# Kernel optimization log

Measured on AMD Instinct MI355X. Metric: run time of the kernel, lower is better.

Reference implementation:

```python
import jax, jax.numpy as jnp
import numpy as np

D_MODEL = 512
N_HEADS = 8
D_K = D_MODEL // N_HEADS


def setup_inputs() -> dict:
    key = jax.random.key(0)
    ks = jax.random.split(key, 11)
    B, L, D = 2, 4096, D_MODEL
    s = 1.0 / np.sqrt(D)
    return {
        "q": jax.random.normal(ks[0], (B, L, D), jnp.float32),
        "k": jax.random.normal(ks[1], (B, L, D), jnp.float32),
        "v": jax.random.normal(ks[2], (B, L, D), jnp.float32),
        "Wq": jax.random.normal(ks[3], (D, D), jnp.float32) * s,
        "bq": jnp.zeros((D,), jnp.float32),
        "Wk": jax.random.normal(ks[4], (D, D), jnp.float32) * s,
        "bk": jnp.zeros((D,), jnp.float32),
        "Wv": jax.random.normal(ks[5], (D, D), jnp.float32) * s,
        "bv": jnp.zeros((D,), jnp.float32),
        "Wo": jax.random.normal(ks[6], (D, D), jnp.float32) * s,
        "bo": jnp.zeros((D,), jnp.float32),
    }


def reference(q, k, v, Wq, bq, Wk, bk, Wv, bv, Wo, bo):
    B, L, D = q.shape
    H, dk = N_HEADS, D_K
    # projections -> [B, H, L, dk]
    qh = (q @ Wq + bq).reshape(B, L, H, dk).transpose(0, 2, 1, 3)
    kh = (k @ Wk + bk).reshape(B, -1, H, dk).transpose(0, 2, 1, 3)
    vh = (v @ Wv + bv).reshape(B, -1, H, dk).transpose(0, 2, 1, 3)
    scores = jnp.einsum("bhqd,bhkd->bhqk", qh, kh) / jnp.sqrt(jnp.float32(dk))
    attn = jax.nn.softmax(scores, axis=-1)  # dropout: eval-mode identity
    ctx = jnp.einsum("bhqk,bhkd->bhqd", attn, vh)
    ctx = ctx.transpose(0, 2, 1, 3).reshape(B, L, D)
    return ctx @ Wo + bo
```

## Files before the change

### kernel.cpp

```cpp
#include <hip/hip_runtime.h>
#include <hip/hip_bf16.h>

#define NB 2
#define NL 4096
#define ND 512
#define NH 8
#define NDK 64
#define NM (NB * NL)
#define QSCALE 0.18033688011112042f

typedef short bf16x8_t __attribute__((ext_vector_type(8)));
typedef float f32x4_t __attribute__((ext_vector_type(4)));

static __device__ __forceinline__ unsigned short f2bs(float f) {
  union { float f; unsigned u; } c; c.f = f;
  unsigned r = c.u + 0x7fffu + ((c.u >> 16) & 1u);
  return (unsigned short)(r >> 16);
}
static __device__ __forceinline__ float bs2f(unsigned short s) {
  union { unsigned u; float f; } c; c.u = ((unsigned)s) << 16; return c.f;
}
static __device__ __forceinline__ unsigned pk_bf16(float a, float b) {
  union { __hip_bfloat162 h; unsigned u; } c;
  c.h = __float22bfloat162_rn(make_float2(a, b));
  return c.u;
}

__global__ __launch_bounds__(256)
void round3_kernel(const float* __restrict__ s0, const float* __restrict__ s1,
                   const float* __restrict__ s2, unsigned short* __restrict__ d0,
                   unsigned short* __restrict__ d1, unsigned short* __restrict__ d2)
{
  const float* s = blockIdx.y == 0 ? s0 : (blockIdx.y == 1 ? s1 : s2);
  unsigned short* d = blockIdx.y == 0 ? d0 : (blockIdx.y == 1 ? d1 : d2);
  const size_t i = ((size_t)blockIdx.x * 256 + threadIdx.x) * 8;
  const float4 f0 = *(const float4*)(s + i);
  const float4 f1 = *(const float4*)(s + i + 4);
  uint4 o;
  o.x = pk_bf16(f0.x, f0.y);
  o.y = pk_bf16(f0.z, f0.w);
  o.z = pk_bf16(f1.x, f1.y);
  o.w = pk_bf16(f1.z, f1.w);
  *(uint4*)(d + i) = o;
}

struct WArgs {
  const float* W[4];
  unsigned short* Th[4];
  unsigned short* Tl[4];
};
__global__ __launch_bounds__(256)
void wsplit_kernel(WArgs a)
{
  const int z = blockIdx.z;
  const float* __restrict__ W = a.W[z];
  const int tid = threadIdx.x;
  const int n = blockIdx.x * 64 + (tid & 63);
  const int kb = blockIdx.y * 64 + (tid >> 6) * 16;
  unsigned short h[16], l[16];
#pragma unroll
  for (int u = 0; u < 16; ++u) {
    const float x = W[(size_t)(kb + u) * ND + n];
    h[u] = f2bs(x);
    l[u] = f2bs(x - bs2f(h[u]));
  }
  unsigned wh[8], wl[8];
#pragma unroll
  for (int p = 0; p < 8; ++p) {
    wh[p] = (unsigned)h[2 * p] | ((unsigned)h[2 * p + 1] << 16);
    wl[p] = (unsigned)l[2 * p] | ((unsigned)l[2 * p + 1] << 16);
  }
  unsigned short* th = a.Th[z] + (size_t)n * ND + kb;
  unsigned short* tl = a.Tl[z] + (size_t)n * ND + kb;
  *(uint4*)th = make_uint4(wh[0], wh[1], wh[2], wh[3]);
  *(uint4*)(th + 8) = make_uint4(wh[4], wh[5], wh[6], wh[7]);
  *(uint4*)tl = make_uint4(wl[0], wl[1], wl[2], wl[3]);
  *(uint4*)(tl + 8) = make_uint4(wl[4], wl[5], wl[6], wl[7]);
}

template <bool ASPLIT, bool HEADOUT>
__device__ __forceinline__ void gemm_core(
    const unsigned short* __restrict__ Ahi, const unsigned short* __restrict__ Alo,
    const unsigned short* __restrict__ Bh, const unsigned short* __restrict__ Bl,
    const float* __restrict__ bias, unsigned short* __restrict__ outH,
    float* __restrict__ outF, int m0, int n0, float scale)
{
  __shared__ unsigned short AH[128][36];
  __shared__ unsigned short AL[ASPLIT ? 128 : 1][36];
  __shared__ unsigned short BHs[128][36];
  __shared__ unsigned short BLs[128][36];

  const int tid = threadIdx.x;
  const int lane = tid & 63, w = tid >> 6;
  const int m = lane & 15, quad = lane >> 4;
  const int r = tid >> 1, hf = (tid & 1) * 16;

  const unsigned short* aRow = Ahi + (size_t)(m0 + r) * ND + hf;
  const unsigned short* alRow = ASPLIT ? (Alo + (size_t)(m0 + r) * ND + hf) : nullptr;
  const unsigned short* bhRow = Bh + (size_t)(n0 + r) * ND + hf;
  const unsigned short* blRow = Bl + (size_t)(n0 + r) * ND + hf;

  uint4 ra0 = *(const uint4*)(aRow);
  uint4 ra1 = *(const uint4*)(aRow + 8);
  uint4 rl0, rl1;
  if constexpr (ASPLIT) {
    rl0 = *(const uint4*)(alRow);
    rl1 = *(const uint4*)(alRow + 8);
  }
  uint4 rbh0 = *(const uint4*)(bhRow);
  uint4 rbh1 = *(const uint4*)(bhRow + 8);
  uint4 rbl0 = *(const uint4*)(blRow);
  uint4 rbl1 = *(const uint4*)(blRow + 8);

  f32x4_t acc[2][8];
#pragma unroll
  for (int i = 0; i < 2; ++i)
#pragma unroll
    for (int j = 0; j < 8; ++j) acc[i][j] = (f32x4_t){0.f, 0.f, 0.f, 0.f};

  for (int k0 = 0; k0 < ND; k0 += 32) {
    __syncthreads();
    *(uint4*)&AH[r][hf] = ra0;
    *(uint4*)&AH[r][hf + 8] = ra1;
    if constexpr (ASPLIT) {
      *(uint4*)&AL[r][hf] = rl0;
      *(uint4*)&AL[r][hf + 8] = rl1;
    }
    *(uint4*)&BHs[r][hf] = rbh0;
    *(uint4*)&BHs[r][hf + 8] = rbh1;
    *(uint4*)&BLs[r][hf] = rbl0;
    *(uint4*)&BLs[r][hf + 8] = rbl1;
    if (k0 + 32 < ND) {
      const int kn = k0 + 32;
      ra0 = *(const uint4*)(aRow + kn);
      ra1 = *(const uint4*)(aRow + kn + 8);
      if constexpr (ASPLIT) {
        rl0 = *(const uint4*)(alRow + kn);
        rl1 = *(const uint4*)(alRow + kn + 8);
      }
      rbh0 = *(const uint4*)(bhRow + kn);
      rbh1 = *(const uint4*)(bhRow + kn + 8);
      rbl0 = *(const uint4*)(blRow + kn);
      rbl1 = *(const uint4*)(blRow + kn + 8);
    }
    __syncthreads();

    bf16x8_t ah[2], al[2];
#pragma unroll
    for (int i = 0; i < 2; ++i) {
      ah[i] = *(const bf16x8_t*)&AH[w * 32 + 16 * i + m][quad * 8];
      if constexpr (ASPLIT) al[i] = *(const bf16x8_t*)&AL[w * 32 + 16 * i + m][quad * 8];
    }
#pragma unroll
    for (int j = 0; j < 8; ++j) {
      const bf16x8_t bhj = *(const bf16x8_t*)&BHs[16 * j + m][quad * 8];
      const bf16x8_t blj = *(const bf16x8_t*)&BLs[16 * j + m][quad * 8];
#pragma unroll
      for (int i = 0; i < 2; ++i) {
        acc[i][j] = __builtin_amdgcn_mfma_f32_16x16x32_bf16(ah[i], bhj, acc[i][j], 0, 0, 0);
        acc[i][j] = __builtin_amdgcn_mfma_f32_16x16x32_bf16(ah[i], blj, acc[i][j], 0, 0, 0);
        if constexpr (ASPLIT)
          acc[i][j] = __builtin_amdgcn_mfma_f32_16x16x32_bf16(al[i], bhj, acc[i][j], 0, 0, 0);
      }
    }
  }

#pragma unroll
  for (int i = 0; i < 2; ++i)
#pragma unroll
    for (int rr = 0; rr < 4; ++rr) {
      const int mg = m0 + w * 32 + 16 * i + quad * 4 + rr;
#pragma unroll
      for (int j = 0; j < 8; ++j) {
        const int n = n0 + 16 * j + m;
        const float c = (acc[i][j][rr] + bias[n]) * scale;
        if constexpr (HEADOUT) {
          const int b = mg >> 12, l = mg & (NL - 1);
          const int h = n >> 6, d = n & (NDK - 1);
          outH[(((size_t)(b * NH + h)) * NL + l) * NDK + d] = f2bs(c);
        } else {
          outF[(size_t)mg * ND + n] = c;
        }
      }
    }
}

struct ProjArgs {
  const unsigned short* A[3];
  const unsigned short* Bh[3];
  const unsigned short* Bl[3];
  const float* bias[3];
  unsigned short* out[3];
  float scale[3];
};
__global__ __launch_bounds__(256, 2)
void gemm_proj_kernel(ProjArgs a)
{
  const int z = blockIdx.z;
  gemm_core<false, true>(a.A[z], nullptr, a.Bh[z], a.Bl[z], a.bias[z], a.out[z],
                         nullptr, blockIdx.x * 128, blockIdx.y * 128, a.scale[z]);
}
__global__ __launch_bounds__(256, 2)
void gemm_out_kernel(const unsigned short* __restrict__ Ahi,
                     const unsigned short* __restrict__ Alo,
                     const unsigned short* __restrict__ Bh,
                     const unsigned short* __restrict__ Bl,
                     const float* __restrict__ bias, float* __restrict__ out)
{
  gemm_core<true, false>(Ahi, Alo, Bh, Bl, bias, nullptr, out,
                         blockIdx.x * 128, blockIdx.y * 128, 1.0f);
}

__global__ __launch_bounds__(256)
void vtrans_kernel(const unsigned short* __restrict__ src, unsigned short* __restrict__ dst)
{
  __shared__ unsigned short T[64][74];
  const int tid = threadIdx.x;
  const int bh = blockIdx.x >> 6;
  const int lt = blockIdx.x & 63;
  const unsigned short* s = src + ((size_t)bh * NL + lt * 64) * NDK;
  const int r = tid >> 2, c = (tid & 3) * 16;
  *(uint4*)&T[r][c] = *(const uint4*)(s + (size_t)r * NDK + c);
  *(uint4*)&T[r][c + 8] = *(const uint4*)(s + (size_t)r * NDK + c + 8);
  __syncthreads();
  const int d = tid >> 2, l0 = (tid & 3) * 16;
  unsigned short e[16];
#pragma unroll
  for (int u = 0; u < 16; ++u) e[u] = T[l0 + u][d];
  uint4 u0, u1;
  u0.x = (unsigned)e[0] | ((unsigned)e[1] << 16);
  u0.y = (unsigned)e[2] | ((unsigned)e[3] << 16);
  u0.z = (unsigned)e[4] | ((unsigned)e[5] << 16);
  u0.w = (unsigned)e[6] | ((unsigned)e[7] << 16);
  u1.x = (unsigned)e[8] | ((unsigned)e[9] << 16);
  u1.y = (unsigned)e[10] | ((unsigned)e[11] << 16);
  u1.z = (unsigned)e[12] | ((unsigned)e[13] << 16);
  u1.w = (unsigned)e[14] | ((unsigned)e[15] << 16);
  unsigned short* dp = dst + (size_t)bh * NDK * NL + (size_t)d * NL + lt * 64 + l0;
  *(uint4*)dp = u0;
  *(uint4*)(dp + 8) = u1;
}

__global__ __launch_bounds__(256, 4)
void attn_kernel(const unsigned short* __restrict__ qh, const unsigned short* __restrict__ kh,
                 const unsigned short* __restrict__ vt_g, float* __restrict__ op,
                 float* __restrict__ lp)
{
  __shared__ unsigned short Ks[64][72];
  __shared__ unsigned short Vt[64][72];
  __shared__ unsigned Pt[64][67];

  const int tid = threadIdx.x;
  const int w = tid >> 6;
  const int lane = tid & 63;
  const int m = lane & 15;
  const int quad = lane >> 4;

  const int bid = blockIdx.x;
  const int half = bid & 1;
  const int qt = (bid >> 1) & 31;
  const int bh = bid >> 6;
  const int kt0 = half * 32, kt1 = kt0 + 32;
  const unsigned short* qb = qh + (size_t)bh * NL * NDK;
  const unsigned short* kb = kh + (size_t)bh * NL * NDK;
  const unsigned short* vb = vt_g + (size_t)bh * NDK * NL;

  bf16x8_t aq[2][2];
#pragma unroll
  for (int mt = 0; mt < 2; ++mt) {
    const unsigned short* qsrc =
        qb + (size_t)(qt * 128 + w * 32 + mt * 16 + m) * NDK + quad * 8;
    aq[mt][0] = *(const bf16x8_t*)(qsrc);
    aq[mt][1] = *(const bf16x8_t*)(qsrc + 32);
  }

  const short ob = (short)0x3F80;
  const bf16x8_t ones = {ob, ob, ob, ob, ob, ob, ob, ob};

  f32x4_t o[2][4];
#pragma unroll
  for (int mt = 0; mt < 2; ++mt)
#pragma unroll
    for (int nt = 0; nt < 4; ++nt) o[mt][nt] = (f32x4_t){0.f, 0.f, 0.f, 0.f};
  f32x4_t ol[2];
  ol[0] = (f32x4_t){0.f, 0.f, 0.f, 0.f};
  ol[1] = (f32x4_t){0.f, 0.f, 0.f, 0.f};

  const int kr = tid >> 2;
  const int kc = (tid & 3) * 16;

  uint4 pk0, pk1, pv0, pv1;
  {
    const unsigned short* ksrc = kb + (size_t)(kt0 * 64 + kr) * NDK + kc;
    pk0 = *(const uint4*)ksrc;
    pk1 = *(const uint4*)(ksrc + 8);
    const unsigned short* vsrc = vb + (size_t)kr * NL + kt0 * 64 + kc;
    pv0 = *(const uint4*)vsrc;
    pv1 = *(const uint4*)(vsrc + 8);
  }

  for (int kt = kt0; kt < kt1; ++kt) {
    __syncthreads();
    *(uint4*)&Ks[kr][kc] = pk0;
    *(uint4*)&Ks[kr][kc + 8] = pk1;
    *(uint4*)&Vt[kr][kc] = pv0;
    *(uint4*)&Vt[kr][kc + 8] = pv1;
    if (kt + 1 < kt1) {
      const unsigned short* ksrc = kb + (size_t)((kt + 1) * 64 + kr) * NDK + kc;
      pk0 = *(const uint4*)ksrc;
      pk1 = *(const uint4*)(ksrc + 8);
      const unsigned short* vsrc = vb + (size_t)kr * NL + (kt + 1) * 64 + kc;
      pv0 = *(const uint4*)vsrc;
      pv1 = *(const uint4*)(vsrc + 8);
    }
    __syncthreads();

#pragma unroll
    for (int nt = 0; nt < 4; ++nt) {
      const bf16x8_t b0 = *(const bf16x8_t*)&Ks[16 * nt + m][quad * 8];
      const bf16x8_t b1 = *(const bf16x8_t*)&Ks[16 * nt + m][quad * 8 + 32];
      f32x4_t s0 = (f32x4_t){0.f, 0.f, 0.f, 0.f};
      s0 = __builtin_amdgcn_mfma_f32_16x16x32_bf16(aq[0][0], b0, s0, 0, 0, 0);
      s0 = __builtin_amdgcn_mfma_f32_16x16x32_bf16(aq[0][1], b1, s0, 0, 0, 0);
      f32x4_t s1 = (f32x4_t){0.f, 0.f, 0.f, 0.f};
      s1 = __builtin_amdgcn_mfma_f32_16x16x32_bf16(aq[1][0], b0, s1, 0, 0, 0);
      s1 = __builtin_amdgcn_mfma_f32_16x16x32_bf16(aq[1][1], b1, s1, 0, 0, 0);
      unsigned pw[4];
#pragma unroll
      for (int r = 0; r < 4; ++r)
        pw[r] = pk_bf16(exp2f(s0[r]), exp2f(s1[r]));
      *(uint4*)&Pt[16 * nt + m][w * 16 + quad * 4] =
          make_uint4(pw[0], pw[1], pw[2], pw[3]);
    }

#pragma unroll
    for (int kb2 = 0; kb2 < 2; ++kb2) {
      unsigned pwv[8];
#pragma unroll
      for (int j = 0; j < 8; ++j)
        pwv[j] = Pt[kb2 * 32 + quad * 8 + j][w * 16 + m];
      union { bf16x8_t v; unsigned d[4]; } pa0, pa1;
#pragma unroll
      for (int t = 0; t < 4; ++t) {
        pa0.d[t] = (pwv[2 * t] & 0xffffu) | (pwv[2 * t + 1] << 16);
        pa1.d[t] = (pwv[2 * t] >> 16) | (pwv[2 * t + 1] & 0xffff0000u);
      }
#pragma unroll
      for (int nt = 0; nt < 4; ++nt) {
        const bf16x8_t vb0 = *(const bf16x8_t*)&Vt[16 * nt + m][kb2 * 32 + quad * 8];
        o[0][nt] = __builtin_amdgcn_mfma_f32_16x16x32_bf16(pa0.v, vb0, o[0][nt], 0, 0, 0);
        o[1][nt] = __builtin_amdgcn_mfma_f32_16x16x32_bf16(pa1.v, vb0, o[1][nt], 0, 0, 0);
      }
      ol[0] = __builtin_amdgcn_mfma_f32_16x16x32_bf16(pa0.v, ones, ol[0], 0, 0, 0);
      ol[1] = __builtin_amdgcn_mfma_f32_16x16x32_bf16(pa1.v, ones, ol[1], 0, 0, 0);
    }
  }

  const size_t pbase = (size_t)(half * 16 + bh) * NL;
#pragma unroll
  for (int mt = 0; mt < 2; ++mt) {
    const int q0 = qt * 128 + w * 32 + mt * 16 + quad * 4;
    if (m == 0)
      *(float4*)&lp[pbase + q0] =
          make_float4(ol[mt][0], ol[mt][1], ol[mt][2], ol[mt][3]);
#pragma unroll
    for (int r = 0; r < 4; ++r) {
      float* dst = op + (pbase + q0 + r) * NDK;
#pragma unroll
      for (int nt = 0; nt < 4; ++nt) dst[16 * nt + m] = o[mt][nt][r];
    }
  }
}

__global__ __launch_bounds__(256)
void merge_kernel(const float* __restrict__ op, const float* __restrict__ lp,
                  unsigned short* __restrict__ ctxh, unsigned short* __restrict__ ctxl)
{
  const size_t t = (size_t)blockIdx.x * 256 + threadIdx.x;
  const int d0 = (int)(t & 7) * 8;
  const size_t row = t >> 3;
  const float l0 = lp[row];
  const float l1 = lp[row + (size_t)16 * NL];
  const float inv = 1.0f / (l0 + l1);
  const float* a = op + row * NDK + d0;
  const float* c = a + (size_t)16 * NL * NDK;
  const float4 a0 = *(const float4*)a, a1 = *(const float4*)(a + 4);
  const float4 c0 = *(const float4*)c, c1 = *(const float4*)(c + 4);
  const float x[8] = {(a0.x + c0.x) * inv, (a0.y + c0.y) * inv,
                      (a0.z + c0.z) * inv, (a0.w + c0.w) * inv,
                      (a1.x + c1.x) * inv, (a1.y + c1.y) * inv,
                      (a1.z + c1.z) * inv, (a1.w + c1.w) * inv};
  unsigned short hs[8], ls[8];
#pragma unroll
  for (int u = 0; u < 8; ++u) {
    hs[u] = f2bs(x[u]);
    ls[u] = f2bs(x[u] - bs2f(hs[u]));
  }
  const int bh = (int)(row >> 12), l = (int)(row & (NL - 1));
  const int b = bh >> 3, h = bh & 7;
  const size_t dst = ((size_t)(b * NL + l)) * ND + h * 64 + d0;
  uint4 uh, ul;
  uh.x = (unsigned)hs[0] | ((unsigned)hs[1] << 16);
  uh.y = (unsigned)hs[2] | ((unsigned)hs[3] << 16);
  uh.z = (unsigned)hs[4] | ((unsigned)hs[5] << 16);
  uh.w = (unsigned)hs[6] | ((unsigned)hs[7] << 16);
  ul.x = (unsigned)ls[0] | ((unsigned)ls[1] << 16);
  ul.y = (unsigned)ls[2] | ((unsigned)ls[3] << 16);
  ul.z = (unsigned)ls[4] | ((unsigned)ls[5] << 16);
  ul.w = (unsigned)ls[6] | ((unsigned)ls[7] << 16);
  *(uint4*)(ctxh + dst) = uh;
  *(uint4*)(ctxl + dst) = ul;
}

extern "C" void kernel_launch(void* const* d_in, const int* in_sizes, int n_in,
                              void* d_out, int out_size, void* d_ws, size_t ws_size,
                              hipStream_t stream)
{
  const float* q  = (const float*)d_in[0];
  const float* k  = (const float*)d_in[1];
  const float* v  = (const float*)d_in[2];
  const float* Wq = (const float*)d_in[3];
  const float* bq = (const float*)d_in[4];
  const float* Wk = (const float*)d_in[5];
  const float* bk = (const float*)d_in[6];
  const float* Wv = (const float*)d_in[7];
  const float* bv = (const float*)d_in[8];
  const float* Wo = (const float*)d_in[9];
  const float* bo = (const float*)d_in[10];

  const size_t PLANE = (size_t)NM * ND;
  unsigned short* wt = (unsigned short*)d_ws;
  unsigned short* qhp = wt + 8 * (size_t)ND * ND;
  unsigned short* khp = qhp + PLANE;
  unsigned short* vtp = khp + PLANE;
  float* op = (float*)(vtp + PLANE);
  float* lp = op + 2 * (size_t)16 * NL * NDK;
  unsigned short* qb = (unsigned short*)op;
  unsigned short* kb = qb + PLANE;
  unsigned short* vb = kb + PLANE;
  unsigned short* vhp_tmp = vb + PLANE;
  unsigned short* ctxh = qhp;
  unsigned short* ctxl = khp;

  unsigned short* wth[4], *wtl[4];
  for (int i = 0; i < 4; ++i) {
    wth[i] = wt + (size_t)(2 * i) * ND * ND;
    wtl[i] = wt + (size_t)(2 * i + 1) * ND * ND;
  }

  round3_kernel<<<dim3(PLANE / (256 * 8), 3), 256, 0, stream>>>(q, k, v, qb, kb, vb);

  WArgs wa;
  wa.W[0] = Wq; wa.W[1] = Wk; wa.W[2] = Wv; wa.W[3] = Wo;
  for (int i = 0; i < 4; ++i) { wa.Th[i] = wth[i]; wa.Tl[i] = wtl[i]; }
  wsplit_kernel<<<dim3(8, 8, 4), 256, 0, stream>>>(wa);

  ProjArgs pa;
  pa.A[0] = qb; pa.A[1] = kb; pa.A[2] = vb;
  pa.Bh[0] = wth[0]; pa.Bl[0] = wtl[0];
  pa.Bh[1] = wth[1]; pa.Bl[1] = wtl[1];
  pa.Bh[2] = wth[2]; pa.Bl[2] = wtl[2];
  pa.bias[0] = bq; pa.bias[1] = bk; pa.bias[2] = bv;
  pa.out[0] = qhp; pa.out[1] = khp; pa.out[2] = vhp_tmp;
  pa.scale[0] = QSCALE; pa.scale[1] = 1.0f; pa.scale[2] = 1.0f;
  gemm_proj_kernel<<<dim3(NM / 128, ND / 128, 3), 256, 0, stream>>>(pa);

  vtrans_kernel<<<dim3(NB * NH * (NL / 64)), 256, 0, stream>>>(vhp_tmp, vtp);

  attn_kernel<<<dim3(NB * NH * (NL / 128) * 2), 256, 0, stream>>>(qhp, khp, vtp, op, lp);

  merge_kernel<<<dim3((16 * NL * NDK) / (256 * 8)), 256, 0, stream>>>(op, lp, ctxh, ctxl);

  gemm_out_kernel<<<dim3(NM / 128, ND / 128), 256, 0, stream>>>(
      ctxh, ctxl, wth[3], wtl[3], bo, (float*)d_out);
}
```

Measured before the change: 288.7 us.

## Fuse V transpose into projection epilogue and shrink output GEMM N-tile

The V projection now writes its result directly in transposed [b,h,d,l] layout through an LDS-staged epilogue, removing the separate vtrans kernel and its extra global round trip. The output GEMM uses a 64-wide N tile, doubling its block count for better CU occupancy on a small grid. Launch bounds are raised to 3 blocks per CU. The staged epilogue adds four barrier-serialized passes per block, and the higher occupancy target may constrain registers.

```diff
diff --git a/kernel.cpp b/kernel.cpp
--- a/kernel.cpp
+++ b/kernel.cpp
@@ -78,7 +78,7 @@
   *(uint4*)(tl + 8) = make_uint4(wl[4], wl[5], wl[6], wl[7]);
 }
 
-template <bool ASPLIT, bool HEADOUT>
+template <bool ASPLIT, int NJ, int OUTMODE>
 __device__ __forceinline__ void gemm_core(
     const unsigned short* __restrict__ Ahi, const unsigned short* __restrict__ Alo,
     const unsigned short* __restrict__ Bh, const unsigned short* __restrict__ Bl,
@@ -87,18 +87,20 @@
 {
   __shared__ unsigned short AH[128][36];
   __shared__ unsigned short AL[ASPLIT ? 128 : 1][36];
-  __shared__ unsigned short BHs[128][36];
-  __shared__ unsigned short BLs[128][36];
+  __shared__ unsigned short BHs[NJ * 16][36];
+  __shared__ unsigned short BLs[NJ * 16][36];
 
   const int tid = threadIdx.x;
   const int lane = tid & 63, w = tid >> 6;
   const int m = lane & 15, quad = lane >> 4;
   const int r = tid >> 1, hf = (tid & 1) * 16;
+  const int rb = (NJ == 8) ? (tid >> 1) : (tid >> 2);
+  const int cb = (NJ == 8) ? ((tid & 1) * 16) : ((tid & 3) * 8);
 
   const unsigned short* aRow = Ahi + (size_t)(m0 + r) * ND + hf;
   const unsigned short* alRow = ASPLIT ? (Alo + (size_t)(m0 + r) * ND + hf) : nullptr;
-  const unsigned short* bhRow = Bh + (size_t)(n0 + r) * ND + hf;
-  const unsigned short* blRow = Bl + (size_t)(n0 + r) * ND + hf;
+  const unsigned short* bhRow = Bh + (size_t)(n0 + rb) * ND + cb;
+  const unsigned short* blRow = Bl + (size_t)(n0 + rb) * ND + cb;
 
   uint4 ra0 = *(const uint4*)(aRow);
   uint4 ra1 = *(const uint4*)(aRow + 8);
@@ -108,15 +110,18 @@
     rl1 = *(const uint4*)(alRow + 8);
   }
   uint4 rbh0 = *(const uint4*)(bhRow);
-  uint4 rbh1 = *(const uint4*)(bhRow + 8);
   uint4 rbl0 = *(const uint4*)(blRow);
-  uint4 rbl1 = *(const uint4*)(blRow + 8);
-
-  f32x4_t acc[2][8];
+  uint4 rbh1, rbl1;
+  if constexpr (NJ == 8) {
+    rbh1 = *(const uint4*)(bhRow + 8);
+    rbl1 = *(const uint4*)(blRow + 8);
+  }
+
+  f32x4_t acc[2][NJ];
 #pragma unroll
   for (int i = 0; i < 2; ++i)
 #pragma unroll
-    for (int j = 0; j < 8; ++j) acc[i][j] = (f32x4_t){0.f, 0.f, 0.f, 0.f};
+    for (int j = 0; j < NJ; ++j) acc[i][j] = (f32x4_t){0.f, 0.f, 0.f, 0.f};
 
   for (int k0 = 0; k0 < ND; k0 += 32) {
     __syncthreads();
@@ -126,10 +131,12 @@
       *(uint4*)&AL[r][hf] = rl0;
       *(uint4*)&AL[r][hf + 8] = rl1;
     }
-    *(uint4*)&BHs[r][hf] = rbh0;
-    *(uint4*)&BHs[r][hf + 8] = rbh1;
-    *(uint4*)&BLs[r][hf] = rbl0;
-    *(uint4*)&BLs[r][hf + 8] = rbl1;
+    *(uint4*)&BHs[rb][cb] = rbh0;
+    *(uint4*)&BLs[rb][cb] = rbl0;
+    if constexpr (NJ == 8) {
+      *(uint4*)&BHs[rb][cb + 8] = rbh1;
+      *(uint4*)&BLs[rb][cb + 8] = rbl1;
+    }
     if (k0 + 32 < ND) {
       const int kn = k0 + 32;
       ra0 = *(const uint4*)(aRow + kn);
@@ -139,9 +146,11 @@
         rl1 = *(const uint4*)(alRow + kn + 8);
       }
       rbh0 = *(const uint4*)(bhRow + kn);
-      rbh1 = *(const uint4*)(bhRow + kn + 8);
       rbl0 = *(const uint4*)(blRow + kn);
-      rbl1 = *(const uint4*)(blRow + kn + 8);
+      if constexpr (NJ == 8) {
+        rbh1 = *(const uint4*)(bhRow + kn + 8);
+        rbl1 = *(const uint4*)(blRow + kn + 8);
+      }
     }
     __syncthreads();
 
@@ -152,7 +161,7 @@
       if constexpr (ASPLIT) al[i] = *(const bf16x8_t*)&AL[w * 32 + 16 * i + m][quad * 8];
     }
 #pragma unroll
-    for (int j = 0; j < 8; ++j) {
+    for (int j = 0; j < NJ; ++j) {
       const bf16x8_t bhj = *(const bf16x8_t*)&BHs[16 * j + m][quad * 8];
       const bf16x8_t blj = *(const bf16x8_t*)&BLs[16 * j + m][quad * 8];
 #pragma unroll
@@ -165,24 +174,59 @@
     }
   }
 
-#pragma unroll
-  for (int i = 0; i < 2; ++i)
-#pragma unroll
-    for (int rr = 0; rr < 4; ++rr) {
-      const int mg = m0 + w * 32 + 16 * i + quad * 4 + rr;
-#pragma unroll
-      for (int j = 0; j < 8; ++j) {
-        const int n = n0 + 16 * j + m;
-        const float c = (acc[i][j][rr] + bias[n]) * scale;
-        if constexpr (HEADOUT) {
-          const int b = mg >> 12, l = mg & (NL - 1);
-          const int h = n >> 6, d = n & (NDK - 1);
-          outH[(((size_t)(b * NH + h)) * NL + l) * NDK + d] = f2bs(c);
-        } else {
-          outF[(size_t)mg * ND + n] = c;
+  if constexpr (OUTMODE != 2) {
+#pragma unroll
+    for (int i = 0; i < 2; ++i)
+#pragma unroll
+      for (int rr = 0; rr < 4; ++rr) {
+        const int mg = m0 + w * 32 + 16 * i + quad * 4 + rr;
+#pragma unroll
+        for (int j = 0; j < NJ; ++j) {
+          const int n = n0 + 16 * j + m;
+          const float c = (acc[i][j][rr] + bias[n]) * scale;
+          if constexpr (OUTMODE == 0) {
+            const int b = mg >> 12, l = mg & (NL - 1);
+            const int h = n >> 6, d = n & (NDK - 1);
+            outH[(((size_t)(b * NH + h)) * NL + l) * NDK + d] = f2bs(c);
+          } else {
+            outF[(size_t)mg * ND + n] = c;
+          }
         }
       }
-    }
+  } else {
+    unsigned short* T = &BHs[0][0];
+    const int bb = m0 >> 12;
+    const int lbase = m0 & (NL - 1);
+#pragma unroll 1
+    for (int p = 0; p < 4; ++p) {
+      __syncthreads();
+      if (w == p) {
+#pragma unroll
+        for (int i = 0; i < 2; ++i)
+#pragma unroll
+          for (int j = 0; j < NJ; ++j) {
+            const int n = 16 * j + m;
+            const float bv = bias[n0 + n];
+            const unsigned w0 = pk_bf16((acc[i][j][0] + bv) * scale,
+                                        (acc[i][j][1] + bv) * scale);
+            const unsigned w1 = pk_bf16((acc[i][j][2] + bv) * scale,
+                                        (acc[i][j][3] + bv) * scale);
+            *(uint2*)&T[n * 34 + 16 * i + quad * 4] = make_uint2(w0, w1);
+          }
+      }
+      __syncthreads();
+      const int n = tid >> 1;
+      const int l0 = (tid & 1) * 16;
+      const uint4 t0 = *(const uint4*)&T[n * 34 + l0];
+      const uint4 t1 = *(const uint4*)&T[n * 34 + l0 + 8];
+      const int ng = n0 + n;
+      const int h = ng >> 6, d = ng & (NDK - 1);
+      unsigned short* dp =
+          outH + (((size_t)(bb * NH + h)) * NDK + d) * NL + lbase + 32 * p + l0;
+      *(uint4*)dp = t0;
+      *(uint4*)(dp + 8) = t1;
+    }
+  }
 }
 
 struct ProjArgs {
@@ -193,52 +237,26 @@
   unsigned short* out[3];
   float scale[3];
 };
-__global__ __launch_bounds__(256, 2)
+__global__ __launch_bounds__(256, 3)
 void gemm_proj_kernel(ProjArgs a)
 {
   const int z = blockIdx.z;
-  gemm_core<false, true>(a.A[z], nullptr, a.Bh[z], a.Bl[z], a.bias[z], a.out[z],
-                         nullptr, blockIdx.x * 128, blockIdx.y * 128, a.scale[z]);
-}
-__global__ __launch_bounds__(256, 2)
+  if (z < 2)
+    gemm_core<false, 8, 0>(a.A[z], nullptr, a.Bh[z], a.Bl[z], a.bias[z], a.out[z],
+                           nullptr, blockIdx.x * 128, blockIdx.y * 128, a.scale[z]);
+  else
+    gemm_core<false, 8, 2>(a.A[2], nullptr, a.Bh[2], a.Bl[2], a.bias[2], a.out[2],
+                           nullptr, blockIdx.x * 128, blockIdx.y * 128, a.scale[2]);
+}
+__global__ __launch_bounds__(256, 3)
 void gemm_out_kernel(const unsigned short* __restrict__ Ahi,
                      const unsigned short* __restrict__ Alo,
                      const unsigned short* __restrict__ Bh,
                      const unsigned short* __restrict__ Bl,
                      const float* __restrict__ bias, float* __restrict__ out)
 {
-  gemm_core<true, false>(Ahi, Alo, Bh, Bl, bias, nullptr, out,
-                         blockIdx.x * 128, blockIdx.y * 128, 1.0f);
-}
-
-__global__ __launch_bounds__(256)
-void vtrans_kernel(const unsigned short* __restrict__ src, unsigned short* __restrict__ dst)
-{
-  __shared__ unsigned short T[64][74];
-  const int tid = threadIdx.x;
-  const int bh = blockIdx.x >> 6;
-  const int lt = blockIdx.x & 63;
-  const unsigned short* s = src + ((size_t)bh * NL + lt * 64) * NDK;
-  const int r = tid >> 2, c = (tid & 3) * 16;
-  *(uint4*)&T[r][c] = *(const uint4*)(s + (size_t)r * NDK + c);
-  *(uint4*)&T[r][c + 8] = *(const uint4*)(s + (size_t)r * NDK + c + 8);
-  __syncthreads();
-  const int d = tid >> 2, l0 = (tid & 3) * 16;
-  unsigned short e[16];
-#pragma unroll
-  for (int u = 0; u < 16; ++u) e[u] = T[l0 + u][d];
-  uint4 u0, u1;
-  u0.x = (unsigned)e[0] | ((unsigned)e[1] << 16);
-  u0.y = (unsigned)e[2] | ((unsigned)e[3] << 16);
-  u0.z = (unsigned)e[4] | ((unsigned)e[5] << 16);
-  u0.w = (unsigned)e[6] | ((unsigned)e[7] << 16);
-  u1.x = (unsigned)e[8] | ((unsigned)e[9] << 16);
-  u1.y = (unsigned)e[10] | ((unsigned)e[11] << 16);
-  u1.z = (unsigned)e[12] | ((unsigned)e[13] << 16);
-  u1.w = (unsigned)e[14] | ((unsigned)e[15] << 16);
-  unsigned short* dp = dst + (size_t)bh * NDK * NL + (size_t)d * NL + lt * 64 + l0;
-  *(uint4*)dp = u0;
-  *(uint4*)(dp + 8) = u1;
+  gemm_core<true, 4, 1>(Ahi, Alo, Bh, Bl, bias, nullptr, out,
+                        blockIdx.x * 128, blockIdx.y * 64, 1.0f);
 }
 
 __global__ __launch_bounds__(256, 4)
@@ -438,7 +456,6 @@
   unsigned short* qb = (unsigned short*)op;
   unsigned short* kb = qb + PLANE;
   unsigned short* vb = kb + PLANE;
-  unsigned short* vhp_tmp = vb + PLANE;
   unsigned short* ctxh = qhp;
   unsigned short* ctxl = khp;
 
@@ -461,16 +478,14 @@
   pa.Bh[1] = wth[1]; pa.Bl[1] = wtl[1];
   pa.Bh[2] = wth[2]; pa.Bl[2] = wtl[2];
   pa.bias[0] = bq; pa.bias[1] = bk; pa.bias[2] = bv;
-  pa.out[0] = qhp; pa.out[1] = khp; pa.out[2] = vhp_tmp;
+  pa.out[0] = qhp; pa.out[1] = khp; pa.out[2] = vtp;
   pa.scale[0] = QSCALE; pa.scale[1] = 1.0f; pa.scale[2] = 1.0f;
   gemm_proj_kernel<<<dim3(NM / 128, ND / 128, 3), 256, 0, stream>>>(pa);
 
-  vtrans_kernel<<<dim3(NB * NH * (NL / 64)), 256, 0, stream>>>(vhp_tmp, vtp);
-
   attn_kernel<<<dim3(NB * NH * (NL / 128) * 2), 256, 0, stream>>>(qhp, khp, vtp, op, lp);
 
   merge_kernel<<<dim3((16 * NL * NDK) / (256 * 8)), 256, 0, stream>>>(op, lp, ctxh, ctxl);
 
-  gemm_out_kernel<<<dim3(NM / 128, ND / 128), 256, 0, stream>>>(
+  gemm_out_kernel<<<dim3(NM / 128, ND / 64), 256, 0, stream>>>(
       ctxh, ctxl, wth[3], wtl[3], bo, (float*)d_out);
 }
```

Result: no change. 285.8 us (-1.0%).
